# Optimization experiments

Measured on AMD Instinct MI355X. Metric: run time of the kernel, lower is better.

Reference implementation:

```python
import jax, jax.numpy as jnp
import numpy as np

B, T, C = 16, 1024, 512
K = 25          # decomp kernel_size
NW = 4          # num_wavelets
SEQ_LEN = T
EPS = 1e-5


def causal_ma(x, k):
    # causal moving average over time with replicate left-pad; x: [B,T,C]
    xp = jnp.pad(x, ((0, 0), (k - 1, 0), (0, 0)), mode='edge')
    cs = jnp.cumsum(xp, axis=1)
    cs0 = jnp.concatenate([jnp.zeros_like(cs[:, :1]), cs], axis=1)
    return (cs0[:, k:] - cs0[:, :-k]) / k


def dwconv3(x, w, b):
    # depthwise conv1d, kernel 3, replicate padding; x: [B,T,C], w: [C,3], b: [C]
    xp = jnp.pad(x, ((0, 0), (1, 1), (0, 0)), mode='edge')
    return xp[:, :-2] * w[:, 0] + xp[:, 1:-1] * w[:, 1] + xp[:, 2:] * w[:, 2] + b


def setup_inputs() -> dict:
    key = jax.random.key(0)
    ks = jax.random.split(key, 12)
    s = 0.02
    return {
        'x': jax.random.normal(ks[0], (B, T, C), dtype=jnp.float32),
        'trend_conv_w': jax.random.normal(ks[1], (C, 3), jnp.float32) * s,
        'trend_conv_b': jnp.zeros((C,), jnp.float32),
        'spike_conv_w': jax.random.normal(ks[2], (C, 3), jnp.float32) * s,
        'spike_conv_b': jnp.zeros((C,), jnp.float32),
        'slope_conv_w': jax.random.normal(ks[3], (C, 3), jnp.float32) * s,
        'slope_conv_b': jnp.zeros((C,), jnp.float32),
        'cheby_coeffs': jax.random.normal(ks[4], (C, C, 4), jnp.float32) * (1.0 / np.sqrt(C * 4)),
        'hyper_w1': jax.random.normal(ks[5], (2 * C, C), jnp.float32) * s,
        'hyper_b1': jnp.zeros((C,), jnp.float32),
        'hyper_w2': jax.random.normal(ks[6], (C, NW * 2), jnp.float32) * s,
        'hyper_b2': jnp.zeros((NW * 2,), jnp.float32),
        'amp_w': jax.random.normal(ks[7], (C, C), jnp.float32) * s,
        'amp_b': jnp.zeros((C,), jnp.float32),
        'wavelet_w': jax.random.normal(ks[8], (NW, C, C), jnp.float32) * (1.0 / np.sqrt(C)),
        'ln_gamma': jnp.ones((C,), jnp.float32),
        'ln_beta': jnp.zeros((C,), jnp.float32),
    }


def reference(x, trend_conv_w, trend_conv_b, spike_conv_w, spike_conv_b,
              slope_conv_w, slope_conv_b, cheby_coeffs,
              hyper_w1, hyper_b1, hyper_w2, hyper_b2,
              amp_w, amp_b, wavelet_w, ln_gamma, ln_beta):
    # --- causal frequency decomposition ---
    trend_part = causal_ma(x, K)              # [B,T,C]
    spike_part = x - trend_part

    # --- depthwise local convs ---
    trend_ctx = dwconv3(trend_part, trend_conv_w, trend_conv_b)
    spike_ctx = dwconv3(spike_part, spike_conv_w, spike_conv_b)

    # --- ChebyKAN on trend (degree 3) ---
    xt = jnp.tanh(trend_ctx)
    basis = jnp.stack([jnp.ones_like(xt), xt, 2 * xt * xt - 1,
                       xt * (4 * xt * xt - 3)], axis=-1)      # [B,T,C,4]
    trend_out = jnp.einsum('btcd,cod->bto', basis, cheby_coeffs)

    # --- hypernetwork for wavelet params ---
    slope = dwconv3(trend_part, slope_conv_w, slope_conv_b)
    slope_pool = slope.mean(axis=1)            # mean over time -> [B,C]
    value_pool = trend_part.mean(axis=1)       # [B,C]
    h = jnp.concatenate([slope_pool, value_pool], axis=-1)
    h = jax.nn.silu(h @ hyper_w1 + hyper_b1)
    params = (h @ hyper_w2 + hyper_b2).reshape(-1, 1, NW, 2)
    dyn_a = jax.nn.softplus(params[..., 0]) + 0.01          # [B,1,NW]
    dyn_b = jax.nn.sigmoid(params[..., 1]) * SEQ_LEN        # [B,1,NW]

    # --- adaptive wavelet KAN on spike ---
    pos = jnp.arange(T, dtype=x.dtype)[None, :, None]       # [1,T,1]
    z = (pos - dyn_b) / dyn_a                               # [B,T,NW]
    psi = (1.0 - z * z) * jnp.exp(-0.5 * z * z)             # Ricker wavelet
    spike_out = jnp.einsum('btw,btc,wco->bto', psi, spike_ctx, wavelet_w)

    # --- amplitude gate, residual, LayerNorm (dropout = identity in eval) ---
    amp_scale = jax.nn.sigmoid(trend_out @ amp_w + amp_b) * 2.0
    out = trend_out + spike_out * amp_scale
    y = out + x
    mu = y.mean(axis=-1, keepdims=True)
    var = ((y - mu) ** 2).mean(axis=-1, keepdims=True)
    return (y - mu) * jax.lax.rsqrt(var + EPS) * ln_gamma + ln_beta
```

## Files before the change

### kernel.cpp

```cpp
#include <hip/hip_runtime.h>
#include <hip/hip_bf16.h>
#include <math.h>

typedef __hip_bfloat16 bf16;
typedef __attribute__((ext_vector_type(8))) short s8v;
typedef __attribute__((ext_vector_type(4))) float f4v;

#define B_   16
#define T_   1024
#define C_   512
#define M_   (B_*T_)
#define NW_  4
#define KWIN 25
#define TCHUNK 16
#define NCHUNK (T_/TCHUNK)

__device__ __forceinline__ float b2f(bf16 v){ return __bfloat162float(v); }
__device__ __forceinline__ bf16  f2b(float v){ return __float2bfloat16(v); }

__device__ __forceinline__ float ftanh(float x){
    float e = __expf(2.f * x);
    return 1.f - 2.f * __builtin_amdgcn_rcpf(e + 1.f);
}
__device__ __forceinline__ float fsig(float x){
    return __builtin_amdgcn_rcpf(1.f + __expf(-x));
}

__device__ __forceinline__ void gload16(const bf16* g, bf16* l) {
    __builtin_amdgcn_global_load_lds(
        (const __attribute__((address_space(1))) void*)g,
        (__attribute__((address_space(3))) void*)l, 16, 0, 0);
}

__global__ __launch_bounds__(256) void front_kernel(
    const float* __restrict__ wav,  const float* __restrict__ ampw,
    const float* __restrict__ cheby, const float* __restrict__ w1,
    const float* __restrict__ x,
    const float* __restrict__ tcw, const float* __restrict__ tcb,
    const float* __restrict__ scw, const float* __restrict__ scb,
    const float* __restrict__ lcw, const float* __restrict__ lcb,
    bf16* __restrict__ WWT, bf16* __restrict__ AWT, bf16* __restrict__ CCT,
    float* __restrict__ bias0_part, float* __restrict__ w1t,
    bf16* __restrict__ xt, bf16* __restrict__ sctx,
    float* __restrict__ slope_part, float* __restrict__ value_part)
{
    const int blk = blockIdx.x;

    if (blk < 2048) {
        __shared__ float t0[32][33], t1[32][33], t2[32][33], t3[32][33];
        const int tx = threadIdx.x & 31, ty = threadIdx.x >> 5;

        if (blk < 1280) {
            const int z = blk >> 8, rem = blk & 255;
            const int ct = (rem & 15) * 32, ot = (rem >> 4) * 32;
            const float* src = (z < 4) ? wav + (size_t)z * 262144 : ampw;
            #pragma unroll
            for (int r = 0; r < 32; r += 8)
                t0[ty + r][tx] = src[(size_t)(ct + ty + r) * 512 + ot + tx];
            __syncthreads();
            #pragma unroll
            for (int r = 0; r < 32; r += 8) {
                int o = ot + ty + r, c = ct + tx;
                bf16 v = f2b(t0[tx][ty + r]);
                if (z < 4) WWT[(size_t)o * 2048 + z * 512 + c] = v;
                else       AWT[(size_t)o * 512 + c] = v;
            }
        } else if (blk < 1536) {
            const int rem = blk - 1280;
            const int ct = (rem & 15) * 32, ot = (rem >> 4) * 32;
            #pragma unroll
            for (int r = 0; r < 32; r += 8) {
                float4 w = *(const float4*)&cheby[(size_t)(ct + ty + r) * 2048 + (size_t)(ot + tx) * 4];
                t0[ty + r][tx] = w.x - w.z;
                t1[ty + r][tx] = w.y - 3.f * w.w;
                t2[ty + r][tx] = 2.f * w.z;
                t3[ty + r][tx] = 4.f * w.w;
            }
            __syncthreads();
            #pragma unroll
            for (int r = 0; r < 32; r += 8) {
                int o = ot + ty + r, c = ct + tx;
                size_t base = (size_t)o * 1536 + c;
                CCT[base]        = f2b(t1[tx][ty + r]);
                CCT[base + 512]  = f2b(t2[tx][ty + r]);
                CCT[base + 1024] = f2b(t3[tx][ty + r]);
            }
            if (threadIdx.x < 32) {
                float s = 0.f;
                #pragma unroll
                for (int cr = 0; cr < 32; ++cr) s += t0[cr][threadIdx.x];
                bias0_part[(size_t)(rem & 15) * 512 + ot + threadIdx.x] = s;
            }
        } else {
            const int rem = blk - 1536;
            const int bo = rem & 15, bj = rem >> 4;
            #pragma unroll
            for (int r = 0; r < 32; r += 8)
                t0[ty + r][tx] = w1[(size_t)(bj * 32 + ty + r) * 512 + bo * 32 + tx];
            __syncthreads();
            #pragma unroll
            for (int r = 0; r < 32; r += 8)
                w1t[(size_t)(bo * 32 + ty + r) * 1024 + bj * 32 + tx] = t0[tx][ty + r];
        }
        return;
    }

    const int dblk  = blk - 2048;
    const int c     = threadIdx.x * 2;
    const int chunk = dblk & 63;
    const int b     = dblk >> 6;
    const int t0i   = chunk * TCHUNK;
    const float* xb = x + (size_t)b * T_ * C_ + c;

    float w0t[2], w1t_[2], w2t[2], bt[2], w0s[2], w1s[2], w2s[2], bs[2], w0l[2], w1l[2], w2l[2], bl[2];
    #pragma unroll
    for (int e = 0; e < 2; ++e) {
        w0t[e]=tcw[(c+e)*3+0]; w1t_[e]=tcw[(c+e)*3+1]; w2t[e]=tcw[(c+e)*3+2]; bt[e]=tcb[c+e];
        w0s[e]=scw[(c+e)*3+0]; w1s[e]=scw[(c+e)*3+1]; w2s[e]=scw[(c+e)*3+2]; bs[e]=scb[c+e];
        w0l[e]=lcw[(c+e)*3+0]; w1l[e]=lcw[(c+e)*3+1]; w2l[e]=lcw[(c+e)*3+2]; bl[e]=lcb[c+e];
    }

    const float inv = 1.f / KWIN;
    float S0 = 0.f, S1 = 0.f;
    float trm[2], tr0[2], xm[2], x0v[2], sAcc[2] = {0.f,0.f}, vAcc[2] = {0.f,0.f};

    auto BODY = [&](int t, float2 an, float2 dn, bool adv) {
        float trp[2], xp[2];
        if (adv) {
            S0 += an.x - dn.x; S1 += an.y - dn.y;
            trp[0] = S0 * inv; trp[1] = S1 * inv;
            xp[0] = an.x; xp[1] = an.y;
        } else {
            trp[0] = tr0[0]; trp[1] = tr0[1];
            xp[0] = x0v[0];  xp[1] = x0v[1];
        }
        union { bf16 h[2]; unsigned u; } u1, usc;
        #pragma unroll
        for (int e = 0; e < 2; ++e) {
            float tctx = w0t[e]*trm[e] + w1t_[e]*tr0[e] + w2t[e]*trp[e] + bt[e];
            float sm = xm[e]-trm[e], s0 = x0v[e]-tr0[e], sp = xp[e]-trp[e];
            float sv = w0s[e]*sm + w1s[e]*s0 + w2s[e]*sp + bs[e];
            float sl = w0l[e]*trm[e] + w1l[e]*tr0[e] + w2l[e]*trp[e] + bl[e];
            sAcc[e] += sl; vAcc[e] += tr0[e];
            u1.h[e] = f2b(ftanh(tctx)); usc.h[e] = f2b(sv);
            trm[e] = tr0[e]; tr0[e] = trp[e]; xm[e] = x0v[e]; x0v[e] = xp[e];
        }
        size_t m = (size_t)b * T_ + t;
        *(unsigned*)&xt[m * C_ + c]   = u1.u;
        *(unsigned*)&sctx[m * C_ + c] = usc.u;
    };

    if (chunk >= 2 && chunk <= NCHUNK - 2) {
        const float* p = xb + (size_t)(t0i - KWIN) * C_;
        #pragma unroll
        for (int i = 0; i < KWIN; ++i) {
            float2 v = *(const float2*)(p + (size_t)i * C_);
            S0 += v.x; S1 += v.y;
        }
        trm[0] = S0 * inv; trm[1] = S1 * inv;
        float2 a = *(const float2*)(p + (size_t)KWIN * C_);
        float2 d = *(const float2*)p;
        S0 += a.x - d.x; S1 += a.y - d.y;
        tr0[0] = S0 * inv; tr0[1] = S1 * inv;
        float2 vm = *(const float2*)(p + (size_t)(KWIN - 1) * C_);
        xm[0] = vm.x; xm[1] = vm.y;
        x0v[0] = a.x; x0v[1] = a.y;

        #pragma unroll
        for (int tt = 0; tt < TCHUNK; ++tt) {
            float2 an = *(const float2*)(p + (size_t)(KWIN + 1 + tt) * C_);
            float2 dn = *(const float2*)(p + (size_t)(1 + tt) * C_);
            BODY(t0i + tt, an, dn, true);
        }
    } else {
        auto X = [&](int i) -> float2 {
            i = i < 0 ? 0 : (i > T_ - 1 ? T_ - 1 : i);
            return *(const float2*)&xb[(size_t)i * C_];
        };
        int j0 = (t0i > 0) ? (t0i - 1) : 0;
        #pragma unroll
        for (int i = j0 - (KWIN - 1); i <= j0; ++i) { float2 v = X(i); S0 += v.x; S1 += v.y; }
        trm[0] = S0 * inv; trm[1] = S1 * inv;
        if (t0i > 0) {
            float2 a = X(t0i), d = X(t0i - KWIN);
            S0 += a.x - d.x; S1 += a.y - d.y;
            tr0[0] = S0 * inv; tr0[1] = S1 * inv;
        } else { tr0[0] = trm[0]; tr0[1] = trm[1]; }
        { float2 v = X(t0i - 1); xm[0] = v.x; xm[1] = v.y; }
        { float2 v = X(t0i);     x0v[0] = v.x; x0v[1] = v.y; }

        #pragma unroll
        for (int tt = 0; tt < TCHUNK; ++tt) {
            int t = t0i + tt, tn = t + 1;
            bool adv = (tn <= T_ - 1);
            float2 an = make_float2(0.f, 0.f), dn = make_float2(0.f, 0.f);
            if (adv) { an = X(tn); dn = X(tn - KWIN); }
            BODY(t, an, dn, adv);
        }
    }
    int pidx = (chunk * B_ + b) * C_ + c;
    *(float2*)&slope_part[pidx] = make_float2(sAcc[0], sAcc[1]);
    *(float2*)&value_part[pidx] = make_float2(vAcc[0], vAcc[1]);
}

__global__ __launch_bounds__(256) void pool_kernel(
    const float* __restrict__ slope_part, const float* __restrict__ value_part,
    const float* __restrict__ bias0_part,
    float* __restrict__ pc, float* __restrict__ bias0)
{
    int idx = blockIdx.x * 256 + threadIdx.x;
    int b = idx >> 10, j = idx & 1023;
    int c = j & 511;
    const float* src = (j < 512) ? slope_part : value_part;
    float s = 0.f;
    #pragma unroll 8
    for (int ch = 0; ch < NCHUNK; ++ch) s += src[(ch * B_ + b) * C_ + c];
    pc[idx] = s * (1.f / T_);
    if (idx < 512) {
        float t = 0.f;
        #pragma unroll
        for (int i = 0; i < 16; ++i) t += bias0_part[(size_t)i * 512 + idx];
        bias0[idx] = t;
    }
}

__global__ __launch_bounds__(256) void hyper1_kernel(
    const float* __restrict__ pc, const float* __restrict__ w1t,
    const float* __restrict__ b1, float* __restrict__ h)
{
    const int o = blockIdx.x, t = threadIdx.x;
    const float4 w = *(const float4*)&w1t[(size_t)o * 1024 + t * 4];
    float acc[16];
    #pragma unroll
    for (int b = 0; b < 16; ++b) {
        float4 p = *(const float4*)&pc[(size_t)b * 1024 + t * 4];
        acc[b] = w.x * p.x + w.y * p.y + w.z * p.z + w.w * p.w;
    }
    #pragma unroll
    for (int off = 32; off >= 1; off >>= 1)
        #pragma unroll
        for (int b = 0; b < 16; ++b) acc[b] += __shfl_down(acc[b], off);
    __shared__ float red[4][16];
    int lane = t & 63, wv = t >> 6;
    if (lane == 0)
        #pragma unroll
        for (int b = 0; b < 16; ++b) red[wv][b] = acc[b];
    __syncthreads();
    if (t < 16) {
        float s = red[0][t] + red[1][t] + red[2][t] + red[3][t] + b1[o];
        h[(size_t)t * 512 + o] = s / (1.f + expf(-s));
    }
}

__global__ __launch_bounds__(128) void hyper2_kernel(
    const float* __restrict__ h, const float* __restrict__ w2,
    const float* __restrict__ b2, float* __restrict__ dyn_a, float* __restrict__ dyn_b)
{
    __shared__ float pp[16][8];
    const int t = threadIdx.x, b = t >> 3, o = t & 7;
    float acc = b2[o];
    #pragma unroll 4
    for (int j = 0; j < 512; ++j) acc += h[(size_t)b * 512 + j] * w2[j * 8 + o];
    pp[b][o] = acc;
    __syncthreads();
    if (t < 64) {
        int bb = t >> 2, w = t & 3;
        float pa = pp[bb][2 * w], pb = pp[bb][2 * w + 1];
        float sp = fmaxf(pa, 0.f) + log1pf(expf(-fabsf(pa)));
        dyn_a[bb * NW_ + w] = sp + 0.01f;
        dyn_b[bb * NW_ + w] = (1.f / (1.f + expf(-pb))) * (float)T_;
    }
}

__global__ __launch_bounds__(512, 4) void gemm_big_kernel(
    const bf16* __restrict__ xt, const bf16* __restrict__ sctxg,
    const bf16* __restrict__ CCT, const bf16* __restrict__ WWT,
    const float* __restrict__ dyn_a, const float* __restrict__ dyn_b,
    const float* __restrict__ bias0,
    bf16* __restrict__ tout, bf16* __restrict__ sout)
{
    __shared__ bf16 lA[128 * 64];
    __shared__ bf16 lB[2][256 * 64];

    const int lin = blockIdx.x;
    const int swz = ((lin & 7) << 6) + (lin >> 3);
    const int mode = swz & 1;
    const int rem = swz >> 1;
    const int nb = rem & 1, mb = rem >> 1;
    const int m0 = mb << 7, n0 = nb << 8;

    const bf16* Ap = mode ? sctxg : xt;
    const bf16* Bp = mode ? WWT : CCT;
    bf16* Cp = mode ? sout : tout;
    const int K = mode ? 2048 : 1536;

    const int tid = threadIdx.x;
    const int lane = tid & 63, wvi = tid >> 6;
    const int wr = wvi >> 2, wc = wvi & 3;
    const int r16 = lane & 15, g = lane >> 4;
    const int row8 = lane >> 3, sl8 = lane & 7;
    const int arow = tid >> 2, quad = tid & 3;

    float4 p4 = make_float4(0.f, 0.f, 0.f, 0.f);
    int ordPacked = 0x210, nIter = 24;
    if (mode) {
        int* wmaxsh = (int*)lA;
        if (tid < 4) wmaxsh[tid] = 0;
        __syncthreads();
        const int bIdx = m0 >> 10;
        const float tpos = (float)((m0 + arow) & 1023);
        float pv[4], am[4];
        #pragma unroll
        for (int w = 0; w < 4; ++w) {
            float z = (tpos - dyn_b[bIdx * 4 + w]) / dyn_a[bIdx * 4 + w];
            float z2 = z * z;
            pv[w] = (1.f - z2) * __expf(-0.5f * z2);
            am[w] = fabsf(pv[w]);
        }
        p4 = make_float4(pv[0], pv[1], pv[2], pv[3]);
        #pragma unroll
        for (int off = 32; off >= 1; off >>= 1)
            #pragma unroll
            for (int w = 0; w < 4; ++w) am[w] = fmaxf(am[w], __shfl_xor(am[w], off));
        if (lane == 0) {
            #pragma unroll
            for (int w = 0; w < 4; ++w) atomicMax(&wmaxsh[w], __float_as_int(am[w]));
        }
        __syncthreads();
        ordPacked = 0; int na = 0;
        #pragma unroll
        for (int w = 0; w < 4; ++w) {
            float f = __int_as_float(__builtin_amdgcn_readfirstlane(wmaxsh[w]));
            if (f > 1e-6f) { ordPacked |= w << (4 * na); ++na; }
        }
        nIter = na * 8;
        __syncthreads();
    }

    auto ktOf = [&](int kidx) -> int {
        int seg = (ordPacked >> ((kidx >> 3) * 4)) & 15;
        return seg * 8 + (kidx & 7);
    };

    const bf16* srcA = Ap + (size_t)(m0 + arow) * 512 + quad * 16;

    f4v acc[4][4];
    #pragma unroll
    for (int i = 0; i < 4; ++i)
        #pragma unroll
        for (int j = 0; j < 4; ++j) acc[i][j] = (f4v)0.f;

    if (nIter > 0) {
        const int ktp = ktOf(0);
        s8v av0 = *(const s8v*)(srcA + ((ktp << 6) & 511));
        s8v av1 = *(const s8v*)(srcA + ((ktp << 6) & 511) + 8);
        #pragma unroll
        for (int c2 = 0; c2 < 4; ++c2) {
            int rb = c2 * 8 + wvi;
            int r = rb * 8 + row8;
            int ls = sl8 ^ (r & 7);
            gload16(Bp + (size_t)(n0 + r) * K + (ktp << 6) + ls * 8, &lB[0][rb * 512]);
        }
        asm volatile("s_waitcnt vmcnt(4)" ::: "memory");

        for (int kidx = 0; kidx < nIter; ++kidx) {
            const int ktc = ktOf(kidx);
            const int wsel = ktc >> 3;
            const float sc = wsel == 0 ? p4.x : wsel == 1 ? p4.y : wsel == 2 ? p4.z : p4.w;

            #pragma unroll
            for (int j2 = 0; j2 < 2; ++j2) {
                s8v a = j2 ? av1 : av0;
                s8v ov;
                if (mode == 0) {
                    if (wsel == 0) ov = a;
                    else {
                        #pragma unroll
                        for (int e = 0; e < 8; ++e) {
                            float v = b2f(((const bf16*)&a)[e]);
                            float vv = v * v;
                            ((bf16*)&ov)[e] = f2b(wsel == 1 ? vv : vv * v);
                        }
                    }
                } else {
                    #pragma unroll
                    for (int e = 0; e < 8; ++e)
                        ((bf16*)&ov)[e] = f2b(b2f(((const bf16*)&a)[e]) * sc);
                }
                int q = quad * 2 + j2;
                *(s8v*)&lA[arow * 64 + ((q ^ (arow & 7)) << 3)] = ov;
            }

            const int kni = (kidx + 1 < nIter) ? kidx + 1 : kidx;
            const int ktn = ktOf(kni);
            const int kOffn = (ktn << 6) & 511;
            av0 = *(const s8v*)(srcA + kOffn);
            av1 = *(const s8v*)(srcA + kOffn + 8);

            {
                const int k0n = ktn << 6;
                bf16* dstB = lB[(kidx + 1) & 1];
                #pragma unroll
                for (int c2 = 0; c2 < 4; ++c2) {
                    int rb = c2 * 8 + wvi;
                    int r = rb * 8 + row8;
                    int ls = sl8 ^ (r & 7);
                    gload16(Bp + (size_t)(n0 + r) * K + k0n + ls * 8, dstB + rb * 512);
                }
            }

            asm volatile("s_waitcnt vmcnt(4) lgkmcnt(0)" ::: "memory");
            asm volatile("s_barrier" ::: "memory");
            __builtin_amdgcn_sched_barrier(0);

            const bf16* lBc = lB[kidx & 1];
            #pragma unroll
            for (int ks = 0; ks < 2; ++ks) {
                s8v afr[4], bfr[4];
                #pragma unroll
                for (int i = 0; i < 4; ++i) {
                    int ar = wr * 64 + i * 16 + r16;
                    afr[i] = *(const s8v*)((const char*)lA + ar * 128 + (((ks * 4 + g) ^ (ar & 7)) << 4));
                }
                #pragma unroll
                for (int j = 0; j < 4; ++j) {
                    int br = wc * 64 + j * 16 + r16;
                    bfr[j] = *(const s8v*)((const char*)lBc + br * 128 + (((ks * 4 + g) ^ (br & 7)) << 4));
                }
                #pragma unroll
                for (int i = 0; i < 4; ++i)
                    #pragma unroll
                    for (int j = 0; j < 4; ++j)
                        acc[i][j] = __builtin_amdgcn_mfma_f32_16x16x32_bf16(afr[i], bfr[j], acc[i][j], 0, 0, 0);
            }

            asm volatile("s_barrier" ::: "memory");
        }

        asm volatile("s_waitcnt vmcnt(0)" ::: "memory");
    }

    #pragma unroll
    for (int i = 0; i < 4; ++i)
        #pragma unroll
        for (int j = 0; j < 4; ++j) {
            int cc = n0 + wc * 64 + j * 16 + r16;
            float bb = (mode == 0) ? bias0[cc] : 0.f;
            #pragma unroll
            for (int r = 0; r < 4; ++r) {
                int rr = m0 + wr * 64 + i * 16 + g * 4 + r;
                Cp[(size_t)rr * 512 + cc] = f2b(acc[i][j][r] + bb);
            }
        }
}

__global__ __launch_bounds__(512, 2) void amp_ln_kernel(
    const bf16* __restrict__ tout, const bf16* __restrict__ sout,
    const bf16* __restrict__ AWT,  const float* __restrict__ ampb,
    const float* __restrict__ x,   const float* __restrict__ gamma,
    const float* __restrict__ beta, float* __restrict__ out)
{
    __shared__ bf16 lA[64 * 64];
    __shared__ bf16 lB[512 * 64];
    __shared__ float red[64 * 16];

    const int m0 = blockIdx.x << 6;
    const int tid = threadIdx.x;
    const int lane = tid & 63, wvi = tid >> 6;
    const int wc = wvi;
    const int r16 = lane & 15, g = lane >> 4;
    const int row8 = lane >> 3, sl8 = lane & 7;

    f4v acc[4][4];
    #pragma unroll
    for (int i = 0; i < 4; ++i)
        #pragma unroll
        for (int j = 0; j < 4; ++j) acc[i][j] = (f4v)0.f;

    for (int kt = 0; kt < 8; ++kt) {
        const int k0 = kt << 6;
        {
            int r = (wvi << 3) + row8;
            int ls = sl8 ^ (r & 7);
            gload16(tout + (size_t)(m0 + r) * 512 + k0 + ls * 8, &lA[wvi * 512]);
        }
        #pragma unroll
        for (int c2 = 0; c2 < 8; ++c2) {
            int r = c2 * 64 + (wvi << 3) + row8;
            int ls = sl8 ^ (r & 7);
            gload16(AWT + (size_t)r * 512 + k0 + ls * 8, &lB[c2 * 4096 + wvi * 512]);
        }
        __syncthreads();
        #pragma unroll
        for (int ks = 0; ks < 2; ++ks) {
            s8v afr[4], bfr[4];
            #pragma unroll
            for (int i = 0; i < 4; ++i) {
                int ar = i * 16 + r16;
                afr[i] = *(const s8v*)((const char*)lA + ar * 128 + (((ks * 4 + g) ^ (ar & 7)) << 4));
            }
            #pragma unroll
            for (int j = 0; j < 4; ++j) {
                int br = wc * 64 + j * 16 + r16;
                bfr[j] = *(const s8v*)((const char*)lB + br * 128 + (((ks * 4 + g) ^ (br & 7)) << 4));
            }
            #pragma unroll
            for (int i = 0; i < 4; ++i)
                #pragma unroll
                for (int j = 0; j < 4; ++j)
                    acc[i][j] = __builtin_amdgcn_mfma_f32_16x16x32_bf16(afr[i], bfr[j], acc[i][j], 0, 0, 0);
        }
        __syncthreads();
    }

    float ab[4], gm[4], bt2[4];
    #pragma unroll
    for (int j = 0; j < 4; ++j) {
        int cc = wc * 64 + j * 16 + r16;
        ab[j] = ampb[cc]; gm[j] = gamma[cc]; bt2[j] = beta[cc];
    }
    f4v s4[4], q4[4];
    #pragma unroll
    for (int i = 0; i < 4; ++i) { s4[i] = (f4v)0.f; q4[i] = (f4v)0.f; }

    #pragma unroll
    for (int i = 0; i < 4; ++i)
        #pragma unroll
        for (int j = 0; j < 4; ++j) {
            int cc = wc * 64 + j * 16 + r16;
            #pragma unroll
            for (int r = 0; r < 4; ++r) {
                size_t rr = (size_t)(m0 + i * 16 + g * 4 + r);
                float amp = 2.f * fsig(acc[i][j][r] + ab[j]);
                float y = b2f(tout[rr * 512 + cc]) + b2f(sout[rr * 512 + cc]) * amp + x[rr * 512 + cc];
                acc[i][j][r] = y;
                s4[i][r] += y; q4[i][r] += y * y;
            }
        }

    #pragma unroll
    for (int off = 1; off < 16; off <<= 1)
        #pragma unroll
        for (int i = 0; i < 4; ++i)
            #pragma unroll
            for (int r = 0; r < 4; ++r) {
                s4[i][r] += __shfl_xor(s4[i][r], off);
                q4[i][r] += __shfl_xor(q4[i][r], off);
            }
    if (r16 == 0) {
        #pragma unroll
        for (int i = 0; i < 4; ++i)
            #pragma unroll
            for (int r = 0; r < 4; ++r) {
                int row = i * 16 + g * 4 + r;
                red[row * 16 + wvi * 2]     = s4[i][r];
                red[row * 16 + wvi * 2 + 1] = q4[i][r];
            }
    }
    __syncthreads();
    if (tid < 64) {
        float ts = 0.f, tq = 0.f;
        #pragma unroll
        for (int w = 0; w < 8; ++w) { ts += red[tid * 16 + w * 2]; tq += red[tid * 16 + w * 2 + 1]; }
        float mu = ts * (1.f / 512.f);
        float var = tq * (1.f / 512.f) - mu * mu;
        red[tid * 16]     = mu;
        red[tid * 16 + 1] = rsqrtf(var + 1e-5f);
    }
    __syncthreads();

    #pragma unroll
    for (int i = 0; i < 4; ++i)
        #pragma unroll
        for (int r = 0; r < 4; ++r) {
            int row = i * 16 + g * 4 + r;
            float mu = red[row * 16], rs = red[row * 16 + 1];
            size_t rr = (size_t)(m0 + row);
            #pragma unroll
            for (int j = 0; j < 4; ++j) {
                int cc = wc * 64 + j * 16 + r16;
                out[rr * 512 + cc] = (acc[i][j][r] - mu) * rs * gm[j] + bt2[j];
            }
        }
}

extern "C" void kernel_launch(void* const* d_in, const int* in_sizes, int n_in,
                              void* d_out, int out_size, void* d_ws, size_t ws_size,
                              hipStream_t stream)
{
    const float* x     = (const float*)d_in[0];
    const float* tcw   = (const float*)d_in[1];
    const float* tcb   = (const float*)d_in[2];
    const float* scw   = (const float*)d_in[3];
    const float* scb   = (const float*)d_in[4];
    const float* lcw   = (const float*)d_in[5];
    const float* lcb   = (const float*)d_in[6];
    const float* cheby = (const float*)d_in[7];
    const float* hw1   = (const float*)d_in[8];
    const float* hb1   = (const float*)d_in[9];
    const float* hw2   = (const float*)d_in[10];
    const float* hb2   = (const float*)d_in[11];
    const float* ampw  = (const float*)d_in[12];
    const float* ampb  = (const float*)d_in[13];
    const float* wav   = (const float*)d_in[14];
    const float* lng   = (const float*)d_in[15];
    const float* lnb   = (const float*)d_in[16];
    float* out = (float*)d_out;

    char* ws = (char*)d_ws;
    size_t off = 0;
    auto alloc = [&](size_t bytes) -> char* {
        char* p = ws + off;
        off += (bytes + 255) & ~(size_t)255;
        return p;
    };
    bf16*  xt         = (bf16*)alloc((size_t)M_ * 512 * 2);
    bf16*  sctx       = (bf16*)alloc((size_t)M_ * 512 * 2);
    bf16*  tout       = (bf16*)alloc((size_t)M_ * 512 * 2);
    bf16*  sout       = (bf16*)alloc((size_t)M_ * 512 * 2);
    bf16*  CCT        = (bf16*)alloc((size_t)512 * 1536 * 2);
    bf16*  WWT        = (bf16*)alloc((size_t)512 * 2048 * 2);
    bf16*  AWT        = (bf16*)alloc((size_t)512 * 512 * 2);
    float* W1T        = (float*)alloc((size_t)512 * 1024 * 4);
    float* bias0_part = (float*)alloc((size_t)16 * 512 * 4);
    float* bias0      = (float*)alloc(512 * 4);
    float* slope_part = (float*)alloc((size_t)NCHUNK * B_ * C_ * 4);
    float* value_part = (float*)alloc((size_t)NCHUNK * B_ * C_ * 4);
    float* pc         = (float*)alloc(B_ * 1024 * 4);
    float* hbuf       = (float*)alloc(B_ * C_ * 4);
    float* dyn_a      = (float*)alloc(B_ * NW_ * 4);
    float* dyn_b      = (float*)alloc(B_ * NW_ * 4);

    front_kernel<<<3072, 256, 0, stream>>>(wav, ampw, cheby, hw1, x,
                                           tcw, tcb, scw, scb, lcw, lcb,
                                           WWT, AWT, CCT, bias0_part, W1T,
                                           xt, sctx, slope_part, value_part);
    pool_kernel<<<64, 256, 0, stream>>>(slope_part, value_part, bias0_part, pc, bias0);
    hyper1_kernel<<<512, 256, 0, stream>>>(pc, W1T, hb1, hbuf);
    hyper2_kernel<<<1, 128, 0, stream>>>(hbuf, hw2, hb2, dyn_a, dyn_b);
    gemm_big_kernel<<<512, 512, 0, stream>>>(xt, sctx, CCT, WWT, dyn_a, dyn_b, bias0, tout, sout);
    amp_ln_kernel<<<256, 512, 0, stream>>>(tout, sout, AWT, ampb, x, lng, lnb, out);
}
```

Baseline: 163.4 us.

## Fold pooling and hypernetwork MLP into the GEMM kernel, dropping three launches

The separate pool, hyper1 and hyper2 kernels are removed, along with the W1 transpose blocks in the front kernel. Each mode-1 block of the big GEMM kernel now sums the per-chunk slope and value partials for its batch, runs the 1024x512 hyper MLP and the 512x8 second layer in LDS, and derives dyn_a and dyn_b itself. Mode-0 blocks sum bias0_part directly in the epilogue. This cuts three kernel launches and their dependency gaps. In exchange, the hypernetwork work (about 0.5M MACs and a 2 MB read of W1) is repeated in every mode-1 block before its GEMM can start.

```diff
diff --git a/kernel.cpp b/kernel.cpp
--- a/kernel.cpp
+++ b/kernel.cpp
@@ -34,19 +34,19 @@
 
 __global__ __launch_bounds__(256) void front_kernel(
     const float* __restrict__ wav,  const float* __restrict__ ampw,
-    const float* __restrict__ cheby, const float* __restrict__ w1,
+    const float* __restrict__ cheby,
     const float* __restrict__ x,
     const float* __restrict__ tcw, const float* __restrict__ tcb,
     const float* __restrict__ scw, const float* __restrict__ scb,
     const float* __restrict__ lcw, const float* __restrict__ lcb,
     bf16* __restrict__ WWT, bf16* __restrict__ AWT, bf16* __restrict__ CCT,
-    float* __restrict__ bias0_part, float* __restrict__ w1t,
+    float* __restrict__ bias0_part,
     bf16* __restrict__ xt, bf16* __restrict__ sctx,
     float* __restrict__ slope_part, float* __restrict__ value_part)
 {
     const int blk = blockIdx.x;
 
-    if (blk < 2048) {
+    if (blk < 1536) {
         __shared__ float t0[32][33], t1[32][33], t2[32][33], t3[32][33];
         const int tx = threadIdx.x & 31, ty = threadIdx.x >> 5;
 
@@ -65,7 +65,7 @@
                 if (z < 4) WWT[(size_t)o * 2048 + z * 512 + c] = v;
                 else       AWT[(size_t)o * 512 + c] = v;
             }
-        } else if (blk < 1536) {
+        } else {
             const int rem = blk - 1280;
             const int ct = (rem & 15) * 32, ot = (rem >> 4) * 32;
             #pragma unroll
@@ -91,21 +91,11 @@
                 for (int cr = 0; cr < 32; ++cr) s += t0[cr][threadIdx.x];
                 bias0_part[(size_t)(rem & 15) * 512 + ot + threadIdx.x] = s;
             }
-        } else {
-            const int rem = blk - 1536;
-            const int bo = rem & 15, bj = rem >> 4;
-            #pragma unroll
-            for (int r = 0; r < 32; r += 8)
-                t0[ty + r][tx] = w1[(size_t)(bj * 32 + ty + r) * 512 + bo * 32 + tx];
-            __syncthreads();
-            #pragma unroll
-            for (int r = 0; r < 32; r += 8)
-                w1t[(size_t)(bo * 32 + ty + r) * 1024 + bj * 32 + tx] = t0[tx][ty + r];
         }
         return;
     }
 
-    const int dblk  = blk - 2048;
+    const int dblk  = blk - 1536;
     const int c     = threadIdx.x * 2;
     const int chunk = dblk & 63;
     const int b     = dblk >> 6;
@@ -203,80 +193,13 @@
     *(float2*)&value_part[pidx] = make_float2(vAcc[0], vAcc[1]);
 }
 
-__global__ __launch_bounds__(256) void pool_kernel(
-    const float* __restrict__ slope_part, const float* __restrict__ value_part,
-    const float* __restrict__ bias0_part,
-    float* __restrict__ pc, float* __restrict__ bias0)
-{
-    int idx = blockIdx.x * 256 + threadIdx.x;
-    int b = idx >> 10, j = idx & 1023;
-    int c = j & 511;
-    const float* src = (j < 512) ? slope_part : value_part;
-    float s = 0.f;
-    #pragma unroll 8
-    for (int ch = 0; ch < NCHUNK; ++ch) s += src[(ch * B_ + b) * C_ + c];
-    pc[idx] = s * (1.f / T_);
-    if (idx < 512) {
-        float t = 0.f;
-        #pragma unroll
-        for (int i = 0; i < 16; ++i) t += bias0_part[(size_t)i * 512 + idx];
-        bias0[idx] = t;
-    }
-}
-
-__global__ __launch_bounds__(256) void hyper1_kernel(
-    const float* __restrict__ pc, const float* __restrict__ w1t,
-    const float* __restrict__ b1, float* __restrict__ h)
-{
-    const int o = blockIdx.x, t = threadIdx.x;
-    const float4 w = *(const float4*)&w1t[(size_t)o * 1024 + t * 4];
-    float acc[16];
-    #pragma unroll
-    for (int b = 0; b < 16; ++b) {
-        float4 p = *(const float4*)&pc[(size_t)b * 1024 + t * 4];
-        acc[b] = w.x * p.x + w.y * p.y + w.z * p.z + w.w * p.w;
-    }
-    #pragma unroll
-    for (int off = 32; off >= 1; off >>= 1)
-        #pragma unroll
-        for (int b = 0; b < 16; ++b) acc[b] += __shfl_down(acc[b], off);
-    __shared__ float red[4][16];
-    int lane = t & 63, wv = t >> 6;
-    if (lane == 0)
-        #pragma unroll
-        for (int b = 0; b < 16; ++b) red[wv][b] = acc[b];
-    __syncthreads();
-    if (t < 16) {
-        float s = red[0][t] + red[1][t] + red[2][t] + red[3][t] + b1[o];
-        h[(size_t)t * 512 + o] = s / (1.f + expf(-s));
-    }
-}
-
-__global__ __launch_bounds__(128) void hyper2_kernel(
-    const float* __restrict__ h, const float* __restrict__ w2,
-    const float* __restrict__ b2, float* __restrict__ dyn_a, float* __restrict__ dyn_b)
-{
-    __shared__ float pp[16][8];
-    const int t = threadIdx.x, b = t >> 3, o = t & 7;
-    float acc = b2[o];
-    #pragma unroll 4
-    for (int j = 0; j < 512; ++j) acc += h[(size_t)b * 512 + j] * w2[j * 8 + o];
-    pp[b][o] = acc;
-    __syncthreads();
-    if (t < 64) {
-        int bb = t >> 2, w = t & 3;
-        float pa = pp[bb][2 * w], pb = pp[bb][2 * w + 1];
-        float sp = fmaxf(pa, 0.f) + log1pf(expf(-fabsf(pa)));
-        dyn_a[bb * NW_ + w] = sp + 0.01f;
-        dyn_b[bb * NW_ + w] = (1.f / (1.f + expf(-pb))) * (float)T_;
-    }
-}
-
 __global__ __launch_bounds__(512, 4) void gemm_big_kernel(
     const bf16* __restrict__ xt, const bf16* __restrict__ sctxg,
     const bf16* __restrict__ CCT, const bf16* __restrict__ WWT,
-    const float* __restrict__ dyn_a, const float* __restrict__ dyn_b,
-    const float* __restrict__ bias0,
+    const float* __restrict__ slope_part, const float* __restrict__ value_part,
+    const float* __restrict__ hw1, const float* __restrict__ hb1,
+    const float* __restrict__ hw2, const float* __restrict__ hb2,
+    const float* __restrict__ bias0_part,
     bf16* __restrict__ tout, bf16* __restrict__ sout)
 {
     __shared__ bf16 lA[128 * 64];
@@ -304,15 +227,48 @@
     float4 p4 = make_float4(0.f, 0.f, 0.f, 0.f);
     int ordPacked = 0x210, nIter = 24;
     if (mode) {
+        float* pcs = (float*)&lB[0][0];
+        float* hsh = pcs + 1024;
+        float* dsh = hsh + 512;
+        const int bIdx = m0 >> 10;
+
+        {
+            float s0 = 0.f, s1 = 0.f;
+            #pragma unroll 8
+            for (int ch = 0; ch < NCHUNK; ++ch) {
+                s0 += slope_part[(size_t)(ch * B_ + bIdx) * 512 + tid];
+                s1 += value_part[(size_t)(ch * B_ + bIdx) * 512 + tid];
+            }
+            pcs[tid]       = s0 * (1.f / T_);
+            pcs[tid + 512] = s1 * (1.f / T_);
+        }
+        __syncthreads();
+        {
+            float acc = hb1[tid];
+            #pragma unroll 4
+            for (int j = 0; j < 1024; ++j)
+                acc += pcs[j] * hw1[(size_t)j * 512 + tid];
+            hsh[tid] = acc * fsig(acc);
+        }
+        __syncthreads();
+        if (tid < 8) {
+            float acc = hb2[tid];
+            for (int j = 0; j < 512; ++j) acc += hsh[j] * hw2[j * 8 + tid];
+            dsh[tid] = acc;
+        }
+        __syncthreads();
+
         int* wmaxsh = (int*)lA;
         if (tid < 4) wmaxsh[tid] = 0;
         __syncthreads();
-        const int bIdx = m0 >> 10;
         const float tpos = (float)((m0 + arow) & 1023);
         float pv[4], am[4];
         #pragma unroll
         for (int w = 0; w < 4; ++w) {
-            float z = (tpos - dyn_b[bIdx * 4 + w]) / dyn_a[bIdx * 4 + w];
+            float pa = dsh[2 * w], pb = dsh[2 * w + 1];
+            float da = fmaxf(pa, 0.f) + log1pf(__expf(-fabsf(pa))) + 0.01f;
+            float db = fsig(pb) * (float)T_;
+            float z = (tpos - db) / da;
             float z2 = z * z;
             pv[w] = (1.f - z2) * __expf(-0.5f * z2);
             am[w] = fabsf(pv[w]);
@@ -445,7 +401,11 @@
         #pragma unroll
         for (int j = 0; j < 4; ++j) {
             int cc = n0 + wc * 64 + j * 16 + r16;
-            float bb = (mode == 0) ? bias0[cc] : 0.f;
+            float bb = 0.f;
+            if (mode == 0) {
+                #pragma unroll
+                for (int p = 0; p < 16; ++p) bb += bias0_part[(size_t)p * 512 + cc];
+            }
             #pragma unroll
             for (int r = 0; r < 4; ++r) {
                 int rr = m0 + wr * 64 + i * 16 + g * 4 + r;
@@ -621,23 +581,17 @@
     bf16*  CCT        = (bf16*)alloc((size_t)512 * 1536 * 2);
     bf16*  WWT        = (bf16*)alloc((size_t)512 * 2048 * 2);
     bf16*  AWT        = (bf16*)alloc((size_t)512 * 512 * 2);
-    float* W1T        = (float*)alloc((size_t)512 * 1024 * 4);
     float* bias0_part = (float*)alloc((size_t)16 * 512 * 4);
-    float* bias0      = (float*)alloc(512 * 4);
     float* slope_part = (float*)alloc((size_t)NCHUNK * B_ * C_ * 4);
     float* value_part = (float*)alloc((size_t)NCHUNK * B_ * C_ * 4);
-    float* pc         = (float*)alloc(B_ * 1024 * 4);
-    float* hbuf       = (float*)alloc(B_ * C_ * 4);
-    float* dyn_a      = (float*)alloc(B_ * NW_ * 4);
-    float* dyn_b      = (float*)alloc(B_ * NW_ * 4);
-
-    front_kernel<<<3072, 256, 0, stream>>>(wav, ampw, cheby, hw1, x,
+
+    front_kernel<<<2560, 256, 0, stream>>>(wav, ampw, cheby, x,
                                            tcw, tcb, scw, scb, lcw, lcb,
-                                           WWT, AWT, CCT, bias0_part, W1T,
+                                           WWT, AWT, CCT, bias0_part,
                                            xt, sctx, slope_part, value_part);
-    pool_kernel<<<64, 256, 0, stream>>>(slope_part, value_part, bias0_part, pc, bias0);
-    hyper1_kernel<<<512, 256, 0, stream>>>(pc, W1T, hb1, hbuf);
-    hyper2_kernel<<<1, 128, 0, stream>>>(hbuf, hw2, hb2, dyn_a, dyn_b);
-    gemm_big_kernel<<<512, 512, 0, stream>>>(xt, sctx, CCT, WWT, dyn_a, dyn_b, bias0, tout, sout);
+    gemm_big_kernel<<<512, 512, 0, stream>>>(xt, sctx, CCT, WWT,
+                                             slope_part, value_part,
+                                             hw1, hb1, hw2, hb2, bias0_part,
+                                             tout, sout);
     amp_ln_kernel<<<256, 512, 0, stream>>>(tout, sout, AWT, ampb, x, lng, lnb, out);
 }
```

After: 202.1 us. 1.24x slower.
